# Performance work log

Measured on AMD Instinct MI355X. Metric: run time of the kernel, lower is better.

The kernel has to match this reference:

```python
import jax, jax.numpy as jnp
import numpy as np

N_NODES = 100000
N_EDGES = 1600000
D_IN = 64
D_OUT = 64


def setup_inputs() -> dict:
    key = jax.random.key(0)
    k1, k2, k3, k4, k5, k6 = jax.random.split(key, 6)
    x = jax.random.normal(k1, (N_NODES, D_IN), dtype=jnp.float32)
    edge_index = jax.random.randint(k2, (2, N_EDGES), 0, N_NODES, dtype=jnp.int64)
    edge_weight = jax.random.uniform(k3, (N_EDGES,), dtype=jnp.float32)
    scale = 1.0 / np.sqrt(D_IN)
    W0 = jax.random.normal(k4, (D_IN, D_OUT), dtype=jnp.float32) * scale
    W1 = jax.random.normal(k5, (D_IN, D_OUT), dtype=jnp.float32) * scale
    b = jax.random.normal(k6, (D_OUT,), dtype=jnp.float32) * 0.01
    return {"x": x, "edge_index": edge_index, "edge_weight": edge_weight,
            "W0": W0, "W1": W1, "b": b}


def reference(x, edge_index, edge_weight, W0, W1, b):
    # ChebConv K=2 with default lambda_max=2.0, sym normalization:
    # L_hat = 2L/lambda_max - I = -D^{-1/2} A D^{-1/2}
    N = x.shape[0]
    row, col = edge_index[0], edge_index[1]
    deg = jax.ops.segment_sum(edge_weight, row, num_segments=N)  # [N]
    deg_safe = jnp.where(deg > 0, deg, 1.0)
    dinv = jnp.where(deg > 0, jax.lax.rsqrt(deg_safe), 0.0)
    norm = -dinv[row] * edge_weight * dinv[col]  # [E], L_hat edge weights
    # Tx_1[i] = sum_{e: col_e = i} norm_e * x[row_e]
    Tx1 = jax.ops.segment_sum(norm[:, None] * x[row], col, num_segments=N)
    # out = lin0(Tx_0) + lin1(Tx_1) + bias
    return x @ W0 + Tx1 @ W1 + b
```

## Files before the change

### kernel.cpp

```cpp
#include <hip/hip_runtime.h>

#define N_NODES 100000
#define N_EDGES 1600000
#define D 64
#define NC 391
#define NCP 392
#define NBLK 128
#define EPB (N_EDGES / NBLK)
#define CAPC 5120
#define SCAP 768
#define AST 68

__device__ __forceinline__ unsigned bf16rne(float f) {
    unsigned u = __float_as_uint(f);
    return (u + 0x7FFFu + ((u >> 16) & 1u)) >> 16;
}
__global__ __launch_bounds__(256) void tobf16_kernel(const float* __restrict__ x,
                                                     ushort* __restrict__ xh,
                                                     float* __restrict__ deg4) {
    int id = blockIdx.x * 256 + threadIdx.x;
    if (id < 4 * N_NODES) deg4[id] = 0.f;
    int i = id * 8;
    float4 a = *(const float4*)(x + i);
    float4 b = *(const float4*)(x + i + 4);
    uint4 o;
    o.x = bf16rne(a.x) | (bf16rne(a.y) << 16);
    o.y = bf16rne(a.z) | (bf16rne(a.w) << 16);
    o.z = bf16rne(b.x) | (bf16rne(b.y) << 16);
    o.w = bf16rne(b.z) | (bf16rne(b.w) << 16);
    *(uint4*)(xh + i) = o;
}

__global__ __launch_bounds__(512) void countA_kernel(const int* __restrict__ row,
                                                     const int* __restrict__ col,
                                                     const float* __restrict__ w,
                                                     float* __restrict__ deg4,
                                                     int* __restrict__ cntA) {
    __shared__ int h[NCP];
    int t = threadIdx.x;
    for (int j = t; j < NCP; j += 512) h[j] = 0;
    __syncthreads();
    int base = blockIdx.x * EPB;
    float* dg = deg4 + (size_t)(blockIdx.x & 3) * N_NODES;
    for (int i = t; i < EPB; i += 512) {
        int e = base + i;
        atomicAdd(&dg[row[e]], w[e]);
        atomicAdd(&h[col[e] >> 8], 1);
    }
    __syncthreads();
    int* mc = cntA + (size_t)blockIdx.x * NCP;
    for (int j = t; j < NCP; j += 512) mc[j] = h[j];
}

__global__ __launch_bounds__(512) void scanA_kernel(int* __restrict__ cntA,
                                                    int* __restrict__ cbase) {
    __shared__ int tot[512];
    int t = threadIdx.x;
    int s = 0;
    if (t < NC)
        for (int b = 0; b < NBLK; ++b) s += cntA[(size_t)b * NCP + t];
    tot[t] = s;
    __syncthreads();
    for (int off = 1; off < 512; off <<= 1) {
        int u = (t >= off) ? tot[t - off] : 0;
        __syncthreads();
        tot[t] += u;
        __syncthreads();
    }
    int excl = (t > 0) ? tot[t - 1] : 0;
    if (t < NC) {
        cbase[t] = excl;
        int off2 = excl;
        for (int b = 0; b < NBLK; ++b) {
            int v = cntA[(size_t)b * NCP + t];
            cntA[(size_t)b * NCP + t] = off2;
            off2 += v;
        }
    }
    if (t == 0) cbase[NC] = N_EDGES;
}

__global__ __launch_bounds__(512) void scatterA_kernel(const int* __restrict__ row,
                                                       const int* __restrict__ col,
                                                       const float* __restrict__ w,
                                                       const int* __restrict__ offA,
                                                       int2* __restrict__ recA) {
    __shared__ int curs[NCP];
    int t = threadIdx.x;
    const int* oa = offA + (size_t)blockIdx.x * NCP;
    for (int j = t; j < NCP; j += 512) curs[j] = oa[j];
    __syncthreads();
    int base = blockIdx.x * EPB;
    for (int i = t; i < EPB; i += 512) {
        int e = base + i;
        int r = row[e];
        int c = col[e];
        float we = w[e];
        int p = atomicAdd(&curs[c >> 8], 1);
        recA[p] = make_int2(((c & 255) << 17) | r, __float_as_int(we));
    }
}

__global__ __launch_bounds__(256) void dinv_kernel(const float* __restrict__ deg4,
                                                   float* __restrict__ dinv) {
    int i = (blockIdx.x * 256 + threadIdx.x) * 4;
    if (i >= N_NODES) return;
    float4 a = *(const float4*)(deg4 + i);
    float4 b = *(const float4*)(deg4 + N_NODES + i);
    float4 c = *(const float4*)(deg4 + 2 * N_NODES + i);
    float4 d = *(const float4*)(deg4 + 3 * N_NODES + i);
    float4 o;
    float sx = a.x + b.x + c.x + d.x;
    float sy = a.y + b.y + c.y + d.y;
    float sz = a.z + b.z + c.z + d.z;
    float sw = a.w + b.w + c.w + d.w;
    o.x = sx > 0.f ? rsqrtf(sx) : 0.f;
    o.y = sy > 0.f ? rsqrtf(sy) : 0.f;
    o.z = sz > 0.f ? rsqrtf(sz) : 0.f;
    o.w = sw > 0.f ? rsqrtf(sw) : 0.f;
    *(float4*)(dinv + i) = o;
}

__global__ __launch_bounds__(256) void sortB_kernel(const int* __restrict__ cbase,
                                                    const float* __restrict__ dinv,
                                                    int2* __restrict__ recA,
                                                    int* __restrict__ node_start) {
    __shared__ int2 buf[CAPC];
    __shared__ int h[256];
    __shared__ int cu[256];
    __shared__ int wsum[4];
    int t = threadIdx.x;
    int cb = blockIdx.x;
    int base = cbase[cb];
    int cnt = min(cbase[cb + 1] - base, CAPC);
    h[t] = 0;
    __syncthreads();
    for (int i = t; i < cnt; i += 256)
        atomicAdd(&h[(recA[base + i].x >> 17) & 255], 1);
    __syncthreads();
    int v = h[t];
    int lane = t & 63, wv = t >> 6;
    int inc = v;
    #pragma unroll
    for (int d2 = 1; d2 < 64; d2 <<= 1) {
        int u = __shfl_up(inc, d2, 64);
        if (lane >= d2) inc += u;
    }
    if (lane == 63) wsum[wv] = inc;
    __syncthreads();
    int woff = 0;
    for (int w2 = 0; w2 < wv; ++w2) woff += wsum[w2];
    int st = woff + inc - v;
    cu[t] = st;
    int nid = cb * 256 + t;
    if (nid <= N_NODES) node_start[nid] = base + st;
    __syncthreads();
    for (int i = t; i < cnt; i += 256) {
        int2 rc = recA[base + i];
        int r = rc.x & 0x1FFFF;
        float cf = __int_as_float(rc.y) * dinv[r];
        int p = atomicAdd(&cu[(rc.x >> 17) & 255], 1);
        buf[p] = make_int2(r, __float_as_int(cf));
    }
    __syncthreads();
    for (int i = t; i < cnt; i += 256) recA[base + i] = buf[i];
}

#define FMA_BF16(e, u)                                                         \
    do { float cc = __int_as_float((e).y);                                     \
        acc0.x += cc * __uint_as_float((u).x << 16);                           \
        acc0.y += cc * __uint_as_float((u).x & 0xFFFF0000u);                   \
        acc0.z += cc * __uint_as_float((u).y << 16);                           \
        acc0.w += cc * __uint_as_float((u).y & 0xFFFF0000u);                   \
        acc1.x += cc * __uint_as_float((u).z << 16);                           \
        acc1.y += cc * __uint_as_float((u).z & 0xFFFF0000u);                   \
        acc1.z += cc * __uint_as_float((u).w << 16);                           \
        acc1.w += cc * __uint_as_float((u).w & 0xFFFF0000u);                   \
    } while (0)

__global__ __launch_bounds__(256, 8) void gather_out_kernel(
        const int2* __restrict__ recS, const int* __restrict__ node_start,
        const float* __restrict__ dinv, const ushort* __restrict__ xh,
        const float* __restrict__ x, const float* __restrict__ W0,
        const float* __restrict__ W1, const float* __restrict__ bias,
        float* __restrict__ out) {
    __shared__ __align__(16) char smemA[32 * AST * 4];
    __shared__ __align__(16) char smemB[32 * AST * 4];
    __shared__ int s33[33];
    int2*  stg = (int2*)smemA;
    float* xs  = (float*)smemA;
    float* ts  = (float*)smemB;

    int tid = threadIdx.x;
    int b   = blockIdx.x;
    int n0  = b * 32;
    int g   = tid >> 3;
    int j   = tid & 7;

    if (tid < 33) s33[tid] = node_start[n0 + tid];
    __syncthreads();
    int base = s33[0];
    int cnt  = s33[32] - base;
    int ks   = s33[g];
    int ke   = s33[g + 1];

    float4 acc0 = make_float4(0.f, 0.f, 0.f, 0.f);
    float4 acc1 = make_float4(0.f, 0.f, 0.f, 0.f);
    const ushort* xhj = xh + (j << 3);

    for (int off = 0; off < cnt; off += SCAP) {
        int m = min(SCAP, cnt - off);
        for (int i = tid; i < m; i += 256) stg[i] = recS[base + off + i];
        __syncthreads();
        int k0 = max(ks - base - off, 0);
        int k1 = min(ke - base - off, m);
        int k = k0;
        for (; k + 3 < k1; k += 4) {
            int2 e0 = stg[k + 0];
            int2 e1 = stg[k + 1];
            int2 e2 = stg[k + 2];
            int2 e3 = stg[k + 3];
            uint4 u0 = *(const uint4*)(xhj + ((size_t)e0.x << 6));
            uint4 u1 = *(const uint4*)(xhj + ((size_t)e1.x << 6));
            uint4 u2 = *(const uint4*)(xhj + ((size_t)e2.x << 6));
            uint4 u3 = *(const uint4*)(xhj + ((size_t)e3.x << 6));
            FMA_BF16(e0, u0);
            FMA_BF16(e1, u1);
            FMA_BF16(e2, u2);
            FMA_BF16(e3, u3);
        }
        for (; k < k1; ++k) {
            int2 e0 = stg[k];
            uint4 u0 = *(const uint4*)(xhj + ((size_t)e0.x << 6));
            FMA_BF16(e0, u0);
        }
        __syncthreads();
    }

    float dn = -dinv[n0 + g];
    float* tp = ts + g * AST + (j << 3);
    *(float4*)tp       = make_float4(dn * acc0.x, dn * acc0.y, dn * acc0.z, dn * acc0.w);
    *(float4*)(tp + 4) = make_float4(dn * acc1.x, dn * acc1.y, dn * acc1.z, dn * acc1.w);
    for (int i = tid; i < 512; i += 256) {
        int nn = i >> 4;
        int kk = (i & 15) << 2;
        *(float4*)&xs[nn * AST + kk] = *(const float4*)(x + (size_t)n0 * D + i * 4);
    }
    __syncthreads();

    int jl = j << 3;
    float4 o0 = *(const float4*)(bias + jl);
    float4 o1 = *(const float4*)(bias + jl + 4);
    for (int k2 = 0; k2 < D; k2 += 4) {
        float4 av = *(const float4*)&xs[g * AST + k2];
        float4 tv = *(const float4*)&ts[g * AST + k2];
        #pragma unroll
        for (int u = 0; u < 4; ++u) {
            float a = (u == 0) ? av.x : (u == 1) ? av.y : (u == 2) ? av.z : av.w;
            float t = (u == 0) ? tv.x : (u == 1) ? tv.y : (u == 2) ? tv.z : tv.w;
            const float4 w00 = *(const float4*)(W0 + (size_t)(k2 + u) * D + jl);
            const float4 w01 = *(const float4*)(W0 + (size_t)(k2 + u) * D + jl + 4);
            const float4 w10 = *(const float4*)(W1 + (size_t)(k2 + u) * D + jl);
            const float4 w11 = *(const float4*)(W1 + (size_t)(k2 + u) * D + jl + 4);
            o0.x += a * w00.x + t * w10.x;
            o0.y += a * w00.y + t * w10.y;
            o0.z += a * w00.z + t * w10.z;
            o0.w += a * w00.w + t * w10.w;
            o1.x += a * w01.x + t * w11.x;
            o1.y += a * w01.y + t * w11.y;
            o1.z += a * w01.z + t * w11.z;
            o1.w += a * w01.w + t * w11.w;
        }
    }
    float* op = out + (size_t)(n0 + g) * D + jl;
    *(float4*)op       = o0;
    *(float4*)(op + 4) = o1;
}

extern "C" void kernel_launch(void* const* d_in, const int* in_sizes, int n_in,
                              void* d_out, int out_size, void* d_ws, size_t ws_size,
                              hipStream_t stream) {
    const float* x    = (const float*)d_in[0];
    const int*   eidx = (const int*)d_in[1];
    const float* ew   = (const float*)d_in[2];
    const float* W0   = (const float*)d_in[3];
    const float* W1   = (const float*)d_in[4];
    const float* b    = (const float*)d_in[5];
    float* out = (float*)d_out;

    const int* row = eidx;
    const int* col = eidx + N_EDGES;

    int2*   recA  = (int2*)d_ws;
    int*    cntA  = (int*)(recA + N_EDGES);
    int*    cbase = cntA + (size_t)NBLK * NCP;
    float*  deg4  = (float*)(cbase + 400);
    float*  dinv  = deg4 + 4 * N_NODES;
    int*    node_start = (int*)(dinv + N_NODES);
    ushort* xh    = (ushort*)(node_start + 100016);

    tobf16_kernel  <<<N_NODES * D / (256 * 8), 256, 0, stream>>>(x, xh, deg4);
    countA_kernel  <<<NBLK, 512, 0, stream>>>(row, col, ew, deg4, cntA);
    scanA_kernel   <<<1, 512, 0, stream>>>(cntA, cbase);
    scatterA_kernel<<<NBLK, 512, 0, stream>>>(row, col, ew, cntA, recA);
    dinv_kernel    <<<(N_NODES / 4 + 255) / 256, 256, 0, stream>>>(deg4, dinv);
    sortB_kernel   <<<NC, 256, 0, stream>>>(cbase, dinv, recA, node_start);
    gather_out_kernel<<<N_NODES / 32, 256, 0, stream>>>(recA, node_start, dinv,
                                                        xh, x, W0, W1, b, out);
}
```

Measured before the change: 340.1 us.

## Replace global degree atomics with LDS range partials and parallelize offset scan

Degree accumulation moves from global float atomics into shared-memory histograms over four node ranges, one per block and edge chunk. Each block writes its partial sums, and dinv reduces them. The serial per-column offset loop in the scan is replaced by a separate kernel doing a parallel wave-shuffle scan per bucket. The gather loop is unrolled to 8 edges with two accumulator sets and masked tails, and the occupancy hint drops from 8 to 5. The partial buffer aliases the record buffer, which scatter overwrites later, and each edge's row and weight are now read four times.

```diff
diff --git a/kernel.cpp b/kernel.cpp
--- a/kernel.cpp
+++ b/kernel.cpp
@@ -6,7 +6,12 @@
 #define NC 391
 #define NCP 392
 #define NBLK 128
-#define EPB (N_EDGES / NBLK)
+#define EPB 12500
+#define RANGES 4
+#define RNG_N 25000
+#define RNG_PAD 25088
+#define CHUNKS 32
+#define EPC 50000
 #define CAPC 5120
 #define SCAP 768
 #define AST 68
@@ -16,11 +21,8 @@
     return (u + 0x7FFFu + ((u >> 16) & 1u)) >> 16;
 }
 __global__ __launch_bounds__(256) void tobf16_kernel(const float* __restrict__ x,
-                                                     ushort* __restrict__ xh,
-                                                     float* __restrict__ deg4) {
-    int id = blockIdx.x * 256 + threadIdx.x;
-    if (id < 4 * N_NODES) deg4[id] = 0.f;
-    int i = id * 8;
+                                                     ushort* __restrict__ xh) {
+    int i = (blockIdx.x * 256 + threadIdx.x) * 8;
     float4 a = *(const float4*)(x + i);
     float4 b = *(const float4*)(x + i + 4);
     uint4 o;
@@ -31,29 +33,21 @@
     *(uint4*)(xh + i) = o;
 }
 
-__global__ __launch_bounds__(512) void countA_kernel(const int* __restrict__ row,
-                                                     const int* __restrict__ col,
-                                                     const float* __restrict__ w,
-                                                     float* __restrict__ deg4,
+__global__ __launch_bounds__(512) void countA_kernel(const int* __restrict__ col,
                                                      int* __restrict__ cntA) {
     __shared__ int h[NCP];
     int t = threadIdx.x;
     for (int j = t; j < NCP; j += 512) h[j] = 0;
     __syncthreads();
     int base = blockIdx.x * EPB;
-    float* dg = deg4 + (size_t)(blockIdx.x & 3) * N_NODES;
-    for (int i = t; i < EPB; i += 512) {
-        int e = base + i;
-        atomicAdd(&dg[row[e]], w[e]);
-        atomicAdd(&h[col[e] >> 8], 1);
-    }
+    for (int i = t; i < EPB; i += 512) atomicAdd(&h[col[base + i] >> 8], 1);
     __syncthreads();
     int* mc = cntA + (size_t)blockIdx.x * NCP;
     for (int j = t; j < NCP; j += 512) mc[j] = h[j];
 }
 
-__global__ __launch_bounds__(512) void scanA_kernel(int* __restrict__ cntA,
-                                                    int* __restrict__ cbase) {
+__global__ __launch_bounds__(512) void scanTot_kernel(const int* __restrict__ cntA,
+                                                      int* __restrict__ cbase) {
     __shared__ int tot[512];
     int t = threadIdx.x;
     int s = 0;
@@ -68,16 +62,70 @@
         __syncthreads();
     }
     int excl = (t > 0) ? tot[t - 1] : 0;
-    if (t < NC) {
-        cbase[t] = excl;
-        int off2 = excl;
-        for (int b = 0; b < NBLK; ++b) {
-            int v = cntA[(size_t)b * NCP + t];
-            cntA[(size_t)b * NCP + t] = off2;
-            off2 += v;
-        }
-    }
+    if (t < NC) cbase[t] = excl;
     if (t == 0) cbase[NC] = N_EDGES;
+}
+
+__global__ __launch_bounds__(128) void scanB_kernel(int* __restrict__ cntA,
+                                                    const int* __restrict__ cbase) {
+    __shared__ int w0tot;
+    int j = blockIdx.x;
+    int t = threadIdx.x;
+    int v = cntA[(size_t)t * NCP + j];
+    int inc = v;
+    #pragma unroll
+    for (int d = 1; d < 64; d <<= 1) {
+        int u = __shfl_up(inc, d, 64);
+        if ((t & 63) >= d) inc += u;
+    }
+    if (t == 63) w0tot = inc;
+    __syncthreads();
+    int off = (t >= 64) ? w0tot : 0;
+    cntA[(size_t)t * NCP + j] = cbase[j] + off + inc - v;
+}
+
+__global__ __launch_bounds__(512) void degpart_kernel(const int* __restrict__ row,
+                                                      const float* __restrict__ w,
+                                                      float* __restrict__ partial) {
+    __shared__ float ldeg[RNG_PAD];
+    int t = threadIdx.x;
+    int r = blockIdx.x >> 5;
+    int c = blockIdx.x & 31;
+    for (int i = t; i < RNG_PAD; i += 512) ldeg[i] = 0.f;
+    __syncthreads();
+    int base  = c * EPC;
+    int rbase = r * RNG_N;
+    for (int i = t; i < EPC; i += 512) {
+        int e = base + i;
+        unsigned d = (unsigned)(row[e] - rbase);
+        float we = w[e];
+        if (d < RNG_N) atomicAdd(&ldeg[d], we);
+    }
+    __syncthreads();
+    float4* dst = (float4*)(partial + (size_t)blockIdx.x * RNG_PAD);
+    const float4* src = (const float4*)ldeg;
+    for (int i = t; i < RNG_PAD / 4; i += 512) dst[i] = src[i];
+}
+
+__global__ __launch_bounds__(256) void dinv_kernel(const float* __restrict__ partial,
+                                                   float* __restrict__ dinv) {
+    int i = (blockIdx.x * 256 + threadIdx.x) * 4;
+    if (i >= N_NODES) return;
+    int r = i / RNG_N;
+    int idx = i - r * RNG_N;
+    const float* p = partial + (size_t)r * CHUNKS * RNG_PAD + idx;
+    float sx = 0.f, sy = 0.f, sz = 0.f, sw = 0.f;
+    #pragma unroll
+    for (int c = 0; c < CHUNKS; ++c) {
+        float4 v = *(const float4*)(p + (size_t)c * RNG_PAD);
+        sx += v.x; sy += v.y; sz += v.z; sw += v.w;
+    }
+    float4 o;
+    o.x = sx > 0.f ? rsqrtf(sx) : 0.f;
+    o.y = sy > 0.f ? rsqrtf(sy) : 0.f;
+    o.z = sz > 0.f ? rsqrtf(sz) : 0.f;
+    o.w = sw > 0.f ? rsqrtf(sw) : 0.f;
+    *(float4*)(dinv + i) = o;
 }
 
 __global__ __launch_bounds__(512) void scatterA_kernel(const int* __restrict__ row,
@@ -101,26 +149,6 @@
     }
 }
 
-__global__ __launch_bounds__(256) void dinv_kernel(const float* __restrict__ deg4,
-                                                   float* __restrict__ dinv) {
-    int i = (blockIdx.x * 256 + threadIdx.x) * 4;
-    if (i >= N_NODES) return;
-    float4 a = *(const float4*)(deg4 + i);
-    float4 b = *(const float4*)(deg4 + N_NODES + i);
-    float4 c = *(const float4*)(deg4 + 2 * N_NODES + i);
-    float4 d = *(const float4*)(deg4 + 3 * N_NODES + i);
-    float4 o;
-    float sx = a.x + b.x + c.x + d.x;
-    float sy = a.y + b.y + c.y + d.y;
-    float sz = a.z + b.z + c.z + d.z;
-    float sw = a.w + b.w + c.w + d.w;
-    o.x = sx > 0.f ? rsqrtf(sx) : 0.f;
-    o.y = sy > 0.f ? rsqrtf(sy) : 0.f;
-    o.z = sz > 0.f ? rsqrtf(sz) : 0.f;
-    o.w = sw > 0.f ? rsqrtf(sw) : 0.f;
-    *(float4*)(dinv + i) = o;
-}
-
 __global__ __launch_bounds__(256) void sortB_kernel(const int* __restrict__ cbase,
                                                     const float* __restrict__ dinv,
                                                     int2* __restrict__ recA,
@@ -166,19 +194,19 @@
     for (int i = t; i < cnt; i += 256) recA[base + i] = buf[i];
 }
 
-#define FMA_BF16(e, u)                                                         \
+#define FMA_BF16T(e, u, A, B)                                                  \
     do { float cc = __int_as_float((e).y);                                     \
-        acc0.x += cc * __uint_as_float((u).x << 16);                           \
-        acc0.y += cc * __uint_as_float((u).x & 0xFFFF0000u);                   \
-        acc0.z += cc * __uint_as_float((u).y << 16);                           \
-        acc0.w += cc * __uint_as_float((u).y & 0xFFFF0000u);                   \
-        acc1.x += cc * __uint_as_float((u).z << 16);                           \
-        acc1.y += cc * __uint_as_float((u).z & 0xFFFF0000u);                   \
-        acc1.z += cc * __uint_as_float((u).w << 16);                           \
-        acc1.w += cc * __uint_as_float((u).w & 0xFFFF0000u);                   \
+        A.x += cc * __uint_as_float((u).x << 16);                              \
+        A.y += cc * __uint_as_float((u).x & 0xFFFF0000u);                      \
+        A.z += cc * __uint_as_float((u).y << 16);                              \
+        A.w += cc * __uint_as_float((u).y & 0xFFFF0000u);                      \
+        B.x += cc * __uint_as_float((u).z << 16);                              \
+        B.y += cc * __uint_as_float((u).z & 0xFFFF0000u);                      \
+        B.z += cc * __uint_as_float((u).w << 16);                              \
+        B.w += cc * __uint_as_float((u).w & 0xFFFF0000u);                      \
     } while (0)
 
-__global__ __launch_bounds__(256, 8) void gather_out_kernel(
+__global__ __launch_bounds__(256, 5) void gather_out_kernel(
         const int2* __restrict__ recS, const int* __restrict__ node_start,
         const float* __restrict__ dinv, const ushort* __restrict__ xh,
         const float* __restrict__ x, const float* __restrict__ W0,
@@ -204,9 +232,12 @@
     int ks   = s33[g];
     int ke   = s33[g + 1];
 
-    float4 acc0 = make_float4(0.f, 0.f, 0.f, 0.f);
-    float4 acc1 = make_float4(0.f, 0.f, 0.f, 0.f);
+    float4 p0 = make_float4(0.f, 0.f, 0.f, 0.f);
+    float4 p1 = make_float4(0.f, 0.f, 0.f, 0.f);
+    float4 q0 = make_float4(0.f, 0.f, 0.f, 0.f);
+    float4 q1 = make_float4(0.f, 0.f, 0.f, 0.f);
     const ushort* xhj = xh + (j << 3);
+    const int2 ez = make_int2(0, 0);
 
     for (int off = 0; off < cnt; off += SCAP) {
         int m = min(SCAP, cnt - off);
@@ -214,28 +245,36 @@
         __syncthreads();
         int k0 = max(ks - base - off, 0);
         int k1 = min(ke - base - off, m);
-        int k = k0;
-        for (; k + 3 < k1; k += 4) {
-            int2 e0 = stg[k + 0];
-            int2 e1 = stg[k + 1];
-            int2 e2 = stg[k + 2];
-            int2 e3 = stg[k + 3];
+        for (int k = k0; k < k1; k += 8) {
+            int2 e0 = stg[k];
+            int2 e1 = (k + 1 < k1) ? stg[k + 1] : ez;
+            int2 e2 = (k + 2 < k1) ? stg[k + 2] : ez;
+            int2 e3 = (k + 3 < k1) ? stg[k + 3] : ez;
+            int2 e4 = (k + 4 < k1) ? stg[k + 4] : ez;
+            int2 e5 = (k + 5 < k1) ? stg[k + 5] : ez;
+            int2 e6 = (k + 6 < k1) ? stg[k + 6] : ez;
+            int2 e7 = (k + 7 < k1) ? stg[k + 7] : ez;
             uint4 u0 = *(const uint4*)(xhj + ((size_t)e0.x << 6));
             uint4 u1 = *(const uint4*)(xhj + ((size_t)e1.x << 6));
             uint4 u2 = *(const uint4*)(xhj + ((size_t)e2.x << 6));
             uint4 u3 = *(const uint4*)(xhj + ((size_t)e3.x << 6));
-            FMA_BF16(e0, u0);
-            FMA_BF16(e1, u1);
-            FMA_BF16(e2, u2);
-            FMA_BF16(e3, u3);
-        }
-        for (; k < k1; ++k) {
-            int2 e0 = stg[k];
-            uint4 u0 = *(const uint4*)(xhj + ((size_t)e0.x << 6));
-            FMA_BF16(e0, u0);
+            uint4 u4 = *(const uint4*)(xhj + ((size_t)e4.x << 6));
+            uint4 u5 = *(const uint4*)(xhj + ((size_t)e5.x << 6));
+            uint4 u6 = *(const uint4*)(xhj + ((size_t)e6.x << 6));
+            uint4 u7 = *(const uint4*)(xhj + ((size_t)e7.x << 6));
+            FMA_BF16T(e0, u0, p0, p1);
+            FMA_BF16T(e1, u1, q0, q1);
+            FMA_BF16T(e2, u2, p0, p1);
+            FMA_BF16T(e3, u3, q0, q1);
+            FMA_BF16T(e4, u4, p0, p1);
+            FMA_BF16T(e5, u5, q0, q1);
+            FMA_BF16T(e6, u6, p0, p1);
+            FMA_BF16T(e7, u7, q0, q1);
         }
         __syncthreads();
     }
+    float4 acc0 = make_float4(p0.x + q0.x, p0.y + q0.y, p0.z + q0.z, p0.w + q0.w);
+    float4 acc1 = make_float4(p1.x + q1.x, p1.y + q1.y, p1.z + q1.z, p1.w + q1.w);
 
     float dn = -dinv[n0 + g];
     float* tp = ts + g * AST + (j << 3);
@@ -291,19 +330,21 @@
     const int* row = eidx;
     const int* col = eidx + N_EDGES;
 
-    int2*   recA  = (int2*)d_ws;
-    int*    cntA  = (int*)(recA + N_EDGES);
-    int*    cbase = cntA + (size_t)NBLK * NCP;
-    float*  deg4  = (float*)(cbase + 400);
-    float*  dinv  = deg4 + 4 * N_NODES;
-    int*    node_start = (int*)(dinv + N_NODES);
-    ushort* xh    = (ushort*)(node_start + 100016);
-
-    tobf16_kernel  <<<N_NODES * D / (256 * 8), 256, 0, stream>>>(x, xh, deg4);
-    countA_kernel  <<<NBLK, 512, 0, stream>>>(row, col, ew, deg4, cntA);
-    scanA_kernel   <<<1, 512, 0, stream>>>(cntA, cbase);
+    float* partial = (float*)d_ws;
+    int2*  recA    = (int2*)d_ws;
+    int*   cntA    = (int*)d_ws + (size_t)NBLK * RNG_PAD;
+    int*   cbase   = cntA + (size_t)NBLK * NCP;
+    float* dinv    = (float*)(cbase + 400);
+    int*   node_start = (int*)(dinv + N_NODES);
+    ushort* xh     = (ushort*)(node_start + 100016);
+
+    tobf16_kernel  <<<N_NODES * D / (256 * 8), 256, 0, stream>>>(x, xh);
+    countA_kernel  <<<NBLK, 512, 0, stream>>>(col, cntA);
+    scanTot_kernel <<<1, 512, 0, stream>>>(cntA, cbase);
+    scanB_kernel   <<<NC, 128, 0, stream>>>(cntA, cbase);
+    degpart_kernel <<<RANGES * CHUNKS, 512, 0, stream>>>(row, ew, partial);
+    dinv_kernel    <<<(N_NODES / 4 + 255) / 256, 256, 0, stream>>>(partial, dinv);
     scatterA_kernel<<<NBLK, 512, 0, stream>>>(row, col, ew, cntA, recA);
-    dinv_kernel    <<<(N_NODES / 4 + 255) / 256, 256, 0, stream>>>(deg4, dinv);
     sortB_kernel   <<<NC, 256, 0, stream>>>(cbase, dinv, recA, node_start);
     gather_out_kernel<<<N_NODES / 32, 256, 0, stream>>>(recA, node_start, dinv,
                                                         xh, x, W0, W1, b, out);
```

Result: faster. 328.1 us (-3.5%).
